# Kernel optimization log

Hardware: AMD Instinct MI355X
Metric: run time of the kernel (lower is better)

## Reference

```python
import jax, jax.numpy as jnp
import numpy as np

D_MODEL = 1024
N_HEADS = 16
HEAD_DIM = D_MODEL // N_HEADS
ROPE_BASE = 10000.0


def setup_inputs() -> dict:
    key = jax.random.key(0)
    ks = jax.random.split(key, 9)
    s = 0.02
    inp = {
        "x": jax.random.normal(ks[0], (2, 2048, D_MODEL), dtype=jnp.float32),
        "Wq": jax.random.normal(ks[1], (D_MODEL, D_MODEL), dtype=jnp.float32) * s,
        "bq": jnp.zeros((D_MODEL,), dtype=jnp.float32),
        "Wk": jax.random.normal(ks[2], (D_MODEL, D_MODEL), dtype=jnp.float32) * s,
        "bk": jnp.zeros((D_MODEL,), dtype=jnp.float32),
        "Wv": jax.random.normal(ks[3], (D_MODEL, D_MODEL), dtype=jnp.float32) * s,
        "bv": jnp.zeros((D_MODEL,), dtype=jnp.float32),
        "Wo": jax.random.normal(ks[4], (D_MODEL, D_MODEL), dtype=jnp.float32) * s,
        "bo": jnp.zeros((D_MODEL,), dtype=jnp.float32),
    }
    return inp


def _rope_cos_sin(T, head_dim, dtype):
    inv_freq = 1.0 / (ROPE_BASE ** (jnp.arange(0, head_dim, 2, dtype=jnp.float32) / head_dim))
    pos = jnp.arange(T, dtype=jnp.float32)
    freqs = jnp.outer(pos, inv_freq)              # [T, head_dim/2]
    emb = jnp.concatenate([freqs, freqs], axis=-1)  # [T, head_dim]
    return jnp.cos(emb).astype(dtype), jnp.sin(emb).astype(dtype)


def _rotate_half(x):
    x1, x2 = jnp.split(x, 2, axis=-1)
    return jnp.concatenate([-x2, x1], axis=-1)


def reference(x, Wq, bq, Wk, bk, Wv, bv, Wo, bo):
    B, T, _ = x.shape
    H, Dh = N_HEADS, HEAD_DIM
    # projections (torch Linear: x @ W.T + b)
    q = (x @ Wq.T + bq).reshape(B, T, H, Dh).transpose(0, 2, 1, 3)  # [B,H,T,Dh]
    k = (x @ Wk.T + bk).reshape(B, T, H, Dh).transpose(0, 2, 1, 3)
    v = (x @ Wv.T + bv).reshape(B, T, H, Dh).transpose(0, 2, 1, 3)
    cos, sin = _rope_cos_sin(T, Dh, x.dtype)  # [T, Dh]
    cos = cos[None, None]
    sin = sin[None, None]
    q = q * cos + _rotate_half(q) * sin
    k = k * cos + _rotate_half(k) * sin
    scale = 1.0 / jnp.sqrt(jnp.asarray(Dh, dtype=x.dtype))
    attn = jnp.einsum("bhqd,bhkd->bhqk", q, k) * scale
    attn = jax.nn.softmax(attn, axis=-1)
    out = jnp.einsum("bhqk,bhkd->bhqd", attn, v)  # [B,H,T,Dh]
    out = out.transpose(0, 2, 1, 3).reshape(B, T, H * Dh)
    return out @ Wo.T + bo
```

## Files before the change

### kernel.cpp

```cpp
#include <hip/hip_runtime.h>
#include <hip/hip_bf16.h>
#include <cstdint>

#define D_MODEL 1024
#define NHEADS 16
#define HDIM 64
#define SEQ 2048
#define NBATCH 2
#define BT (NBATCH * SEQ)

typedef short bf16x8 __attribute__((ext_vector_type(8)));
typedef float f32x4 __attribute__((ext_vector_type(4)));
typedef unsigned short u16;
typedef unsigned int u32;

__device__ inline u16 f2bf(float f) {
    union { float f; u32 u; } x;
    x.f = f;
    u32 r = (x.u + 0x7fffu + ((x.u >> 16) & 1u)) >> 16;
    return (u16)r;
}

__device__ inline u32 pack2bf(float a, float b) {
    union { float f; u32 u; } x, y;
    x.f = a; y.f = b;
    return ((x.u + 0x8000u) >> 16) | ((y.u + 0x8000u) & 0xffff0000u);
}

__device__ inline void async_copy16(const u16* g, u16* l) {
    __builtin_amdgcn_global_load_lds((const __attribute__((address_space(1))) void*)g,
                                     (__attribute__((address_space(3))) void*)l, 16, 0, 0);
}

#define X4 (BT * D_MODEL / 4)
#define W4 (D_MODEL * D_MODEL / 4)
#define ROPE_N (SEQ * 32)

__global__ void prep_kernel(const float* __restrict__ x,
                            const float* __restrict__ wq, const float* __restrict__ wk,
                            const float* __restrict__ wv, const float* __restrict__ wo,
                            u16* __restrict__ xb,
                            u16* __restrict__ dq, u16* __restrict__ dk,
                            u16* __restrict__ dv, u16* __restrict__ dow,
                            float* __restrict__ cosT, float* __restrict__ sinT) {
    int idx = blockIdx.x * blockDim.x + threadIdx.x;
    if (idx < X4) {
        float4 v = ((const float4*)x)[idx];
        ushort4 o;
        o.x = f2bf(v.x); o.y = f2bf(v.y); o.z = f2bf(v.z); o.w = f2bf(v.w);
        ((ushort4*)xb)[idx] = o;
    } else if (idx < X4 + 4 * W4) {
        int j = idx - X4;
        int w = j >> 18, i = j & (W4 - 1);
        const float* s = (w == 0) ? wq : (w == 1) ? wk : (w == 2) ? wv : wo;
        u16* d = (w == 0) ? dq : (w == 1) ? dk : (w == 2) ? dv : dow;
        float4 v = ((const float4*)s)[i];
        ushort4 o;
        o.x = f2bf(v.x); o.y = f2bf(v.y); o.z = f2bf(v.z); o.w = f2bf(v.w);
        ((ushort4*)d)[i] = o;
    } else {
        int j = idx - (X4 + 4 * W4);
        if (j < ROPE_N) {
            int t = j >> 5, dd = j & 31;
            float invf = exp2f(-(float)dd * (13.287712379549449f / 32.0f));
            float ang = (float)t * invf;
            float s, c;
            sincosf(ang, &s, &c);
            cosT[t * HDIM + dd] = c;      cosT[t * HDIM + dd + 32] = c;
            sinT[t * HDIM + dd] = s;      sinT[t * HDIM + dd + 32] = s;
        }
    }
}

__device__ inline void gemm_tile_core(const u16* __restrict__ A, const u16* __restrict__ Bw,
                                      int blkM, int blkN,
                                      u16* Asmem, u16* Bsmem, f32x4 acc[4][4]) {
    const int tid = threadIdx.x;
    const int lane = tid & 63;
    const int wave = tid >> 6;
    const int waveM = wave >> 1, waveN = wave & 1;
    const int quad = lane >> 4, l16 = lane & 15;

    const int srow = tid >> 2;
    const int scol = (tid & 3) << 3;
    const u16* Ag0 = A + (size_t)(blkM * 128 + srow) * D_MODEL + scol;
    const u16* Ag1 = Ag0 + (size_t)64 * D_MODEL;
    const u16* Bg0 = Bw + (size_t)(blkN * 128 + srow) * D_MODEL + scol;
    const u16* Bg1 = Bg0 + (size_t)64 * D_MODEL;
    u16* Al0 = Asmem + srow * 32 + scol;
    u16* Al1 = Al0 + 64 * 32;
    u16* Bl0 = Bsmem + srow * 32 + scol;
    u16* Bl1 = Bl0 + 64 * 32;

    for (int k0 = 0; k0 < D_MODEL; k0 += 32) {
        __syncthreads();
        async_copy16(Ag0 + k0, Al0);
        async_copy16(Ag1 + k0, Al1);
        async_copy16(Bg0 + k0, Bl0);
        async_copy16(Bg1 + k0, Bl1);
        __syncthreads();
        bf16x8 af[4], bfr[4];
#pragma unroll
        for (int mt = 0; mt < 4; ++mt)
            af[mt] = *(const bf16x8*)&Asmem[(waveM * 64 + mt * 16 + l16) * 32 + quad * 8];
#pragma unroll
        for (int nt = 0; nt < 4; ++nt)
            bfr[nt] = *(const bf16x8*)&Bsmem[(waveN * 64 + nt * 16 + l16) * 32 + quad * 8];
#pragma unroll
        for (int mt = 0; mt < 4; ++mt)
#pragma unroll
            for (int nt = 0; nt < 4; ++nt)
                acc[mt][nt] = __builtin_amdgcn_mfma_f32_16x16x32_bf16(af[mt], bfr[nt], acc[mt][nt], 0, 0, 0);
    }
}

#define QSCALE 0.1803368801111204f

__global__ __launch_bounds__(256) void gemm_qkv_kernel(
    const u16* __restrict__ xb,
    const u16* __restrict__ wqb, const u16* __restrict__ wkb, const u16* __restrict__ wvb,
    const float* __restrict__ bq, const float* __restrict__ bk, const float* __restrict__ bv,
    const float* __restrict__ cosT, const float* __restrict__ sinT,
    u16* __restrict__ Qb, u16* __restrict__ Kb, u16* __restrict__ VTb) {
    __shared__ __align__(16) u16 Asmem[128 * 32];
    __shared__ __align__(16) u16 Bsmem[128 * 32];
    const int z = blockIdx.z;
    const u16* Bw = (z == 0) ? wqb : (z == 1) ? wkb : wvb;
    const float* bias = (z == 0) ? bq : (z == 1) ? bk : bv;

    f32x4 acc[4][4];
#pragma unroll
    for (int mt = 0; mt < 4; ++mt)
#pragma unroll
        for (int nt = 0; nt < 4; ++nt)
            acc[mt][nt] = (f32x4){0.f, 0.f, 0.f, 0.f};

    gemm_tile_core(xb, Bw, blockIdx.x, blockIdx.y, Asmem, Bsmem, acc);

    const int lane = threadIdx.x & 63, wave = threadIdx.x >> 6;
    const int waveM = wave >> 1, waveN = wave & 1;
    const int quad = lane >> 4, l16 = lane & 15;
    const int gm0 = blockIdx.x * 128 + waveM * 64 + quad * 4;
    const int gn0 = blockIdx.y * 128 + waveN * 64 + l16;

    float bvv[4];
#pragma unroll
    for (int nt = 0; nt < 4; ++nt) bvv[nt] = bias[gn0 + nt * 16];
#pragma unroll
    for (int mt = 0; mt < 4; ++mt)
#pragma unroll
        for (int nt = 0; nt < 4; ++nt)
#pragma unroll
            for (int r = 0; r < 4; ++r) acc[mt][nt][r] += bvv[nt];

    if (z < 2) {
        u16* dst = (z == 0) ? Qb : Kb;
        const float post = (z == 0) ? QSCALE : 1.0f;
#pragma unroll
        for (int mt = 0; mt < 4; ++mt) {
#pragma unroll
            for (int nt = 0; nt < 4; ++nt) {
                int n = gn0 + nt * 16;
                int d = n & 63, h = n >> 6;
#pragma unroll
                for (int r = 0; r < 4; ++r) {
                    int gm = gm0 + mt * 16 + r;
                    int t = gm & (SEQ - 1), b = gm >> 11;
                    float c = cosT[t * HDIM + d], s = sinT[t * HDIM + d];
                    float part = acc[mt][nt ^ 2][r];
                    float rot = (d < 32) ? -part : part;
                    float val = (acc[mt][nt][r] * c + rot * s) * post;
                    dst[((b * NHEADS + h) * SEQ + t) * HDIM + d] = f2bf(val);
                }
            }
        }
    } else {
#pragma unroll
        for (int mt = 0; mt < 4; ++mt) {
            int gm = gm0 + mt * 16;
            int t0 = gm & (SEQ - 1), b = gm >> 11;
#pragma unroll
            for (int nt = 0; nt < 4; ++nt) {
                int n = gn0 + nt * 16;
                int d = n & 63, h = n >> 6;
                uint2 w;
                w.x = pack2bf(acc[mt][nt][0], acc[mt][nt][1]);
                w.y = pack2bf(acc[mt][nt][2], acc[mt][nt][3]);
                *(uint2*)&VTb[((size_t)(b * NHEADS + h) * HDIM + d) * SEQ + t0] = w;
            }
        }
    }
}

#define LPAD 72

__global__ __launch_bounds__(256) void flash_kernel(
    const u16* __restrict__ Qb, const u16* __restrict__ Kb, const u16* __restrict__ VTb,
    u16* __restrict__ attn) {
    __shared__ __align__(16) u16 Ks[64 * LPAD];
    __shared__ __align__(16) u16 VTs[64 * LPAD];
    __shared__ __align__(16) u16 Ps[4][32 * LPAD];

    const int tid = threadIdx.x;
    const int wave = tid >> 6, lane = tid & 63;
    const int quad = lane >> 4, l16 = lane & 15;
    const int bh = blockIdx.y;
    const u16* Qh = Qb + (size_t)bh * SEQ * HDIM;
    const u16* Kh = Kb + (size_t)bh * SEQ * HDIM;
    const u16* Vh = VTb + (size_t)bh * HDIM * SEQ;
    const int qblk = blockIdx.x * 128 + wave * 32;
    u16* Pw = (u16*)Ps[wave];

    bf16x8 aq[2][2];
#pragma unroll
    for (int nt2 = 0; nt2 < 2; ++nt2)
#pragma unroll
        for (int ks = 0; ks < 2; ++ks)
            aq[nt2][ks] = *(const bf16x8*)&Qh[(qblk + nt2 * 16 + l16) * HDIM + ks * 32 + quad * 8];

    f32x4 o[2][4];
    float lsum[2] = {0.f, 0.f};
#pragma unroll
    for (int mt2 = 0; mt2 < 2; ++mt2)
#pragma unroll
        for (int nt = 0; nt < 4; ++nt) o[mt2][nt] = (f32x4){0.f, 0.f, 0.f, 0.f};

    const int lr = tid >> 2;
    const int lc = (tid & 3) * 16;

    for (int kt = 0; kt < SEQ / 64; ++kt) {
        __syncthreads();
        *(int4*)&Ks[lr * LPAD + lc] = *(const int4*)&Kh[(kt * 64 + lr) * HDIM + lc];
        *(int4*)&Ks[lr * LPAD + lc + 8] = *(const int4*)&Kh[(kt * 64 + lr) * HDIM + lc + 8];
        *(int4*)&VTs[lr * LPAD + lc] = *(const int4*)&Vh[lr * SEQ + kt * 64 + lc];
        *(int4*)&VTs[lr * LPAD + lc + 8] = *(const int4*)&Vh[lr * SEQ + kt * 64 + lc + 8];
        __syncthreads();

        f32x4 sacc[4][2];
#pragma unroll
        for (int mt = 0; mt < 4; ++mt)
#pragma unroll
            for (int nt2 = 0; nt2 < 2; ++nt2) sacc[mt][nt2] = (f32x4){0.f, 0.f, 0.f, 0.f};
#pragma unroll
        for (int ks = 0; ks < 2; ++ks) {
            bf16x8 kf[4];
#pragma unroll
            for (int mt = 0; mt < 4; ++mt)
                kf[mt] = *(const bf16x8*)&Ks[(mt * 16 + l16) * LPAD + ks * 32 + quad * 8];
#pragma unroll
            for (int mt = 0; mt < 4; ++mt)
#pragma unroll
                for (int nt2 = 0; nt2 < 2; ++nt2)
                    sacc[mt][nt2] = __builtin_amdgcn_mfma_f32_16x16x32_bf16(kf[mt], aq[nt2][ks], sacc[mt][nt2], 0, 0, 0);
        }

#pragma unroll
        for (int mt = 0; mt < 4; ++mt) {
#pragma unroll
            for (int nt2 = 0; nt2 < 2; ++nt2) {
                float p0 = __builtin_amdgcn_exp2f(fminf(sacc[mt][nt2][0], 60.0f));
                float p1 = __builtin_amdgcn_exp2f(fminf(sacc[mt][nt2][1], 60.0f));
                float p2 = __builtin_amdgcn_exp2f(fminf(sacc[mt][nt2][2], 60.0f));
                float p3 = __builtin_amdgcn_exp2f(fminf(sacc[mt][nt2][3], 60.0f));
                lsum[nt2] += (p0 + p1) + (p2 + p3);
                uint2 w;
                w.x = pack2bf(p0, p1);
                w.y = pack2bf(p2, p3);
                *(uint2*)&Pw[(nt2 * 16 + l16) * LPAD + mt * 16 + quad * 4] = w;
            }
        }

#pragma unroll
        for (int ks = 0; ks < 2; ++ks) {
            bf16x8 pf[2], vf[4];
#pragma unroll
            for (int mt2 = 0; mt2 < 2; ++mt2)
                pf[mt2] = *(const bf16x8*)&Pw[(mt2 * 16 + l16) * LPAD + ks * 32 + quad * 8];
#pragma unroll
            for (int nt = 0; nt < 4; ++nt)
                vf[nt] = *(const bf16x8*)&VTs[(nt * 16 + l16) * LPAD + ks * 32 + quad * 8];
#pragma unroll
            for (int mt2 = 0; mt2 < 2; ++mt2)
#pragma unroll
                for (int nt = 0; nt < 4; ++nt)
                    o[mt2][nt] = __builtin_amdgcn_mfma_f32_16x16x32_bf16(pf[mt2], vf[nt], o[mt2][nt], 0, 0, 0);
        }
    }

#pragma unroll
    for (int nt2 = 0; nt2 < 2; ++nt2) {
        lsum[nt2] += __shfl_xor(lsum[nt2], 16, 64);
        lsum[nt2] += __shfl_xor(lsum[nt2], 32, 64);
    }
    float rinv[2][4];
#pragma unroll
    for (int mt2 = 0; mt2 < 2; ++mt2)
#pragma unroll
        for (int r = 0; r < 4; ++r)
            rinv[mt2][r] = 1.0f / __shfl(lsum[mt2], quad * 4 + r, 64);

    const int b = bh >> 4, h = bh & 15;
#pragma unroll
    for (int mt2 = 0; mt2 < 2; ++mt2) {
#pragma unroll
        for (int nt = 0; nt < 4; ++nt) {
            int d = nt * 16 + l16;
#pragma unroll
            for (int r = 0; r < 4; ++r) {
                int q = qblk + mt2 * 16 + quad * 4 + r;
                attn[((size_t)(b * SEQ + q)) * D_MODEL + h * HDIM + d] = f2bf(o[mt2][nt][r] * rinv[mt2][r]);
            }
        }
    }
}

__global__ __launch_bounds__(256) void gemm_out_kernel(
    const u16* __restrict__ attn, const u16* __restrict__ wob,
    const float* __restrict__ bo, float* __restrict__ dout) {
    __shared__ __align__(16) u16 Asmem[128 * 32];
    __shared__ __align__(16) u16 Bsmem[128 * 32];

    f32x4 acc[4][4];
#pragma unroll
    for (int mt = 0; mt < 4; ++mt)
#pragma unroll
        for (int nt = 0; nt < 4; ++nt) acc[mt][nt] = (f32x4){0.f, 0.f, 0.f, 0.f};

    gemm_tile_core(attn, wob, blockIdx.x, blockIdx.y, Asmem, Bsmem, acc);

    const int lane = threadIdx.x & 63, wave = threadIdx.x >> 6;
    const int waveM = wave >> 1, waveN = wave & 1;
    const int quad = lane >> 4, l16 = lane & 15;
    const int gm0 = blockIdx.x * 128 + waveM * 64 + quad * 4;
    const int gn0 = blockIdx.y * 128 + waveN * 64 + l16;

    float bvv[4];
#pragma unroll
    for (int nt = 0; nt < 4; ++nt) bvv[nt] = bo[gn0 + nt * 16];
#pragma unroll
    for (int mt = 0; mt < 4; ++mt)
#pragma unroll
        for (int nt = 0; nt < 4; ++nt)
#pragma unroll
            for (int r = 0; r < 4; ++r)
                dout[(size_t)(gm0 + mt * 16 + r) * D_MODEL + gn0 + nt * 16] = acc[mt][nt][r] + bvv[nt];
}

extern "C" void kernel_launch(void* const* d_in, const int* in_sizes, int n_in,
                              void* d_out, int out_size, void* d_ws, size_t ws_size,
                              hipStream_t stream) {
    const float* x  = (const float*)d_in[0];
    const float* Wq = (const float*)d_in[1];
    const float* bq = (const float*)d_in[2];
    const float* Wk = (const float*)d_in[3];
    const float* bk = (const float*)d_in[4];
    const float* Wv = (const float*)d_in[5];
    const float* bv = (const float*)d_in[6];
    const float* Wo = (const float*)d_in[7];
    const float* bo = (const float*)d_in[8];
    float* dout = (float*)d_out;

    char* ws = (char*)d_ws;
    size_t off = 0;
    u16* xb  = (u16*)(ws + off); off += (size_t)BT * D_MODEL * 2;
    u16* wqb = (u16*)(ws + off); off += (size_t)D_MODEL * D_MODEL * 2;
    u16* wkb = (u16*)(ws + off); off += (size_t)D_MODEL * D_MODEL * 2;
    u16* wvb = (u16*)(ws + off); off += (size_t)D_MODEL * D_MODEL * 2;
    u16* wob = (u16*)(ws + off); off += (size_t)D_MODEL * D_MODEL * 2;
    u16* Qb  = (u16*)(ws + off); off += (size_t)BT * D_MODEL * 2;
    u16* Kb  = (u16*)(ws + off); off += (size_t)BT * D_MODEL * 2;
    u16* VTb = (u16*)(ws + off); off += (size_t)BT * D_MODEL * 2;
    u16* attn = (u16*)(ws + off); off += (size_t)BT * D_MODEL * 2;
    float* cosT = (float*)(ws + off); off += (size_t)SEQ * HDIM * 4;
    float* sinT = (float*)(ws + off); off += (size_t)SEQ * HDIM * 4;

    const int prepN = X4 + 4 * W4 + ROPE_N;
    prep_kernel<<<dim3((prepN + 255) / 256), 256, 0, stream>>>(
        x, Wq, Wk, Wv, Wo, xb, wqb, wkb, wvb, wob, cosT, sinT);
    gemm_qkv_kernel<<<dim3(BT / 128, D_MODEL / 128, 3), 256, 0, stream>>>(
        xb, wqb, wkb, wvb, bq, bk, bv, cosT, sinT, Qb, Kb, VTb);
    flash_kernel<<<dim3(SEQ / 128, NBATCH * NHEADS), 256, 0, stream>>>(Qb, Kb, VTb, attn);
    gemm_out_kernel<<<dim3(BT / 128, D_MODEL / 128), 256, 0, stream>>>(attn, wob, bo, dout);
}
```

Before: 229.6 us.

## Shrink flash and output-GEMM blocks, compute row sums via MFMA

The flash kernel now runs 64 queries per 128-thread block instead of 128 per 256, which doubles the grid to improve occupancy and SM coverage. The softmax denominator is computed by an MFMA against a ones vector instead of per-lane adds plus shuffles. pack2bf switches to the HIP RNE intrinsic. The output GEMM uses 64x128 tiles with its own async-copy loop, doubling the block count. The cost is more redundant K/V loads per query, one extra MFMA per P tile, and the row sums now come from bf16-rounded P.

```diff
diff --git a/kernel.cpp b/kernel.cpp
--- a/kernel.cpp
+++ b/kernel.cpp
@@ -22,9 +22,9 @@
 }
 
 __device__ inline u32 pack2bf(float a, float b) {
-    union { float f; u32 u; } x, y;
-    x.f = a; y.f = b;
-    return ((x.u + 0x8000u) >> 16) | ((y.u + 0x8000u) & 0xffff0000u);
+    union { __hip_bfloat162 h; u32 u; } c;
+    c.h = __float22bfloat162_rn(float2{a, b});
+    return c.u;
 }
 
 __device__ inline void async_copy16(const u16* g, u16* l) {
@@ -194,12 +194,12 @@
 
 #define LPAD 72
 
-__global__ __launch_bounds__(256) void flash_kernel(
+__global__ __launch_bounds__(128) void flash_kernel(
     const u16* __restrict__ Qb, const u16* __restrict__ Kb, const u16* __restrict__ VTb,
     u16* __restrict__ attn) {
     __shared__ __align__(16) u16 Ks[64 * LPAD];
     __shared__ __align__(16) u16 VTs[64 * LPAD];
-    __shared__ __align__(16) u16 Ps[4][32 * LPAD];
+    __shared__ __align__(16) u16 Ps[2][32 * LPAD];
 
     const int tid = threadIdx.x;
     const int wave = tid >> 6, lane = tid & 63;
@@ -208,8 +208,12 @@
     const u16* Qh = Qb + (size_t)bh * SEQ * HDIM;
     const u16* Kh = Kb + (size_t)bh * SEQ * HDIM;
     const u16* Vh = VTb + (size_t)bh * HDIM * SEQ;
-    const int qblk = blockIdx.x * 128 + wave * 32;
+    const int qblk = blockIdx.x * 64 + wave * 32;
     u16* Pw = (u16*)Ps[wave];
+
+    bf16x8 ones;
+#pragma unroll
+    for (int i = 0; i < 8; ++i) ones[i] = (short)0x3F80;
 
     bf16x8 aq[2][2];
 #pragma unroll
@@ -218,22 +222,24 @@
         for (int ks = 0; ks < 2; ++ks)
             aq[nt2][ks] = *(const bf16x8*)&Qh[(qblk + nt2 * 16 + l16) * HDIM + ks * 32 + quad * 8];
 
-    f32x4 o[2][4];
-    float lsum[2] = {0.f, 0.f};
-#pragma unroll
-    for (int mt2 = 0; mt2 < 2; ++mt2)
+    f32x4 o[2][4], accL[2];
+#pragma unroll
+    for (int mt2 = 0; mt2 < 2; ++mt2) {
+        accL[mt2] = (f32x4){0.f, 0.f, 0.f, 0.f};
 #pragma unroll
         for (int nt = 0; nt < 4; ++nt) o[mt2][nt] = (f32x4){0.f, 0.f, 0.f, 0.f};
-
-    const int lr = tid >> 2;
-    const int lc = (tid & 3) * 16;
+    }
+
+    const int lr = tid >> 1;
+    const int lc = (tid & 1) * 32;
 
     for (int kt = 0; kt < SEQ / 64; ++kt) {
         __syncthreads();
-        *(int4*)&Ks[lr * LPAD + lc] = *(const int4*)&Kh[(kt * 64 + lr) * HDIM + lc];
-        *(int4*)&Ks[lr * LPAD + lc + 8] = *(const int4*)&Kh[(kt * 64 + lr) * HDIM + lc + 8];
-        *(int4*)&VTs[lr * LPAD + lc] = *(const int4*)&Vh[lr * SEQ + kt * 64 + lc];
-        *(int4*)&VTs[lr * LPAD + lc + 8] = *(const int4*)&Vh[lr * SEQ + kt * 64 + lc + 8];
+#pragma unroll
+        for (int j = 0; j < 4; ++j) {
+            *(int4*)&Ks[lr * LPAD + lc + j * 8] = *(const int4*)&Kh[(kt * 64 + lr) * HDIM + lc + j * 8];
+            *(int4*)&VTs[lr * LPAD + lc + j * 8] = *(const int4*)&Vh[lr * SEQ + kt * 64 + lc + j * 8];
+        }
         __syncthreads();
 
         f32x4 sacc[4][2];
@@ -262,7 +268,6 @@
                 float p1 = __builtin_amdgcn_exp2f(fminf(sacc[mt][nt2][1], 60.0f));
                 float p2 = __builtin_amdgcn_exp2f(fminf(sacc[mt][nt2][2], 60.0f));
                 float p3 = __builtin_amdgcn_exp2f(fminf(sacc[mt][nt2][3], 60.0f));
-                lsum[nt2] += (p0 + p1) + (p2 + p3);
                 uint2 w;
                 w.x = pack2bf(p0, p1);
                 w.y = pack2bf(p2, p3);
@@ -280,24 +285,21 @@
             for (int nt = 0; nt < 4; ++nt)
                 vf[nt] = *(const bf16x8*)&VTs[(nt * 16 + l16) * LPAD + ks * 32 + quad * 8];
 #pragma unroll
-            for (int mt2 = 0; mt2 < 2; ++mt2)
+            for (int mt2 = 0; mt2 < 2; ++mt2) {
 #pragma unroll
                 for (int nt = 0; nt < 4; ++nt)
                     o[mt2][nt] = __builtin_amdgcn_mfma_f32_16x16x32_bf16(pf[mt2], vf[nt], o[mt2][nt], 0, 0, 0);
-        }
-    }
-
-#pragma unroll
-    for (int nt2 = 0; nt2 < 2; ++nt2) {
-        lsum[nt2] += __shfl_xor(lsum[nt2], 16, 64);
-        lsum[nt2] += __shfl_xor(lsum[nt2], 32, 64);
-    }
+                accL[mt2] = __builtin_amdgcn_mfma_f32_16x16x32_bf16(pf[mt2], ones, accL[mt2], 0, 0, 0);
+            }
+        }
+    }
+
     float rinv[2][4];
 #pragma unroll
     for (int mt2 = 0; mt2 < 2; ++mt2)
 #pragma unroll
         for (int r = 0; r < 4; ++r)
-            rinv[mt2][r] = 1.0f / __shfl(lsum[mt2], quad * 4 + r, 64);
+            rinv[mt2][r] = 1.0f / accL[mt2][r];
 
     const int b = bh >> 4, h = bh & 15;
 #pragma unroll
@@ -317,28 +319,57 @@
 __global__ __launch_bounds__(256) void gemm_out_kernel(
     const u16* __restrict__ attn, const u16* __restrict__ wob,
     const float* __restrict__ bo, float* __restrict__ dout) {
-    __shared__ __align__(16) u16 Asmem[128 * 32];
+    __shared__ __align__(16) u16 Asmem[64 * 32];
     __shared__ __align__(16) u16 Bsmem[128 * 32];
 
-    f32x4 acc[4][4];
-#pragma unroll
-    for (int mt = 0; mt < 4; ++mt)
-#pragma unroll
-        for (int nt = 0; nt < 4; ++nt) acc[mt][nt] = (f32x4){0.f, 0.f, 0.f, 0.f};
-
-    gemm_tile_core(attn, wob, blockIdx.x, blockIdx.y, Asmem, Bsmem, acc);
-
-    const int lane = threadIdx.x & 63, wave = threadIdx.x >> 6;
+    const int tid = threadIdx.x;
+    const int lane = tid & 63, wave = tid >> 6;
     const int waveM = wave >> 1, waveN = wave & 1;
     const int quad = lane >> 4, l16 = lane & 15;
-    const int gm0 = blockIdx.x * 128 + waveM * 64 + quad * 4;
+
+    f32x4 acc[2][4];
+#pragma unroll
+    for (int mt = 0; mt < 2; ++mt)
+#pragma unroll
+        for (int nt = 0; nt < 4; ++nt) acc[mt][nt] = (f32x4){0.f, 0.f, 0.f, 0.f};
+
+    const int srow = tid >> 2;
+    const int scol = (tid & 3) << 3;
+    const u16* Ag = attn + (size_t)(blockIdx.x * 64 + srow) * D_MODEL + scol;
+    const u16* Bg0 = wob + (size_t)(blockIdx.y * 128 + srow) * D_MODEL + scol;
+    const u16* Bg1 = Bg0 + (size_t)64 * D_MODEL;
+    u16* Al = Asmem + srow * 32 + scol;
+    u16* Bl0 = Bsmem + srow * 32 + scol;
+    u16* Bl1 = Bl0 + 64 * 32;
+
+    for (int k0 = 0; k0 < D_MODEL; k0 += 32) {
+        __syncthreads();
+        async_copy16(Ag + k0, Al);
+        async_copy16(Bg0 + k0, Bl0);
+        async_copy16(Bg1 + k0, Bl1);
+        __syncthreads();
+        bf16x8 af[2], bfr[4];
+#pragma unroll
+        for (int mt = 0; mt < 2; ++mt)
+            af[mt] = *(const bf16x8*)&Asmem[(waveM * 32 + mt * 16 + l16) * 32 + quad * 8];
+#pragma unroll
+        for (int nt = 0; nt < 4; ++nt)
+            bfr[nt] = *(const bf16x8*)&Bsmem[(waveN * 64 + nt * 16 + l16) * 32 + quad * 8];
+#pragma unroll
+        for (int mt = 0; mt < 2; ++mt)
+#pragma unroll
+            for (int nt = 0; nt < 4; ++nt)
+                acc[mt][nt] = __builtin_amdgcn_mfma_f32_16x16x32_bf16(af[mt], bfr[nt], acc[mt][nt], 0, 0, 0);
+    }
+
+    const int gm0 = blockIdx.x * 64 + waveM * 32 + quad * 4;
     const int gn0 = blockIdx.y * 128 + waveN * 64 + l16;
 
     float bvv[4];
 #pragma unroll
     for (int nt = 0; nt < 4; ++nt) bvv[nt] = bo[gn0 + nt * 16];
 #pragma unroll
-    for (int mt = 0; mt < 4; ++mt)
+    for (int mt = 0; mt < 2; ++mt)
 #pragma unroll
         for (int nt = 0; nt < 4; ++nt)
 #pragma unroll
@@ -379,6 +410,6 @@
         x, Wq, Wk, Wv, Wo, xb, wqb, wkb, wvb, wob, cosT, sinT);
     gemm_qkv_kernel<<<dim3(BT / 128, D_MODEL / 128, 3), 256, 0, stream>>>(
         xb, wqb, wkb, wvb, bq, bk, bv, cosT, sinT, Qb, Kb, VTb);
-    flash_kernel<<<dim3(SEQ / 128, NBATCH * NHEADS), 256, 0, stream>>>(Qb, Kb, VTb, attn);
-    gemm_out_kernel<<<dim3(BT / 128, D_MODEL / 128), 256, 0, stream>>>(attn, wob, bo, dout);
-}
+    flash_kernel<<<dim3(SEQ / 64, NBATCH * NHEADS), 128, 0, stream>>>(Qb, Kb, VTb, attn);
+    gemm_out_kernel<<<dim3(BT / 64, D_MODEL / 128), 256, 0, stream>>>(attn, wob, bo, dout);
+}
```

After: 256.0 us. 11.5% more time.
